# Optimization experiments

Measured on AMD Instinct MI355X. Metric: run time of the kernel, lower is better.

The kernel has to match this reference:

```python
import jax, jax.numpy as jnp
import numpy as np

N_NODES = 100000
IN_C, HID_C, OUT_C = 128, 128, 64
N_EDGES, N_POS, N_NEG = 1600000, 200000, 200000
BN_EPS = 1e-5


def setup_inputs() -> dict:
    key = jax.random.key(0)
    ks = jax.random.split(key, 24)
    s = 0.05
    inp = {
        'x': jax.random.normal(ks[0], (N_NODES, IN_C), jnp.float32),
        'edge_index': jax.random.randint(ks[1], (2, N_EDGES), 0, N_NODES, jnp.int64 if jax.config.jax_enable_x64 else jnp.int32),
        'pos_edge_index': jax.random.randint(ks[2], (2, N_POS), 0, N_NODES, jnp.int32),
        'neg_edge_index': jax.random.randint(ks[3], (2, N_NEG), 0, N_NODES, jnp.int32),
        # SAGEConv layer 1 (in->hid): lin_l (bias) on aggregated neighbors, lin_r (no bias) on root
        'Wl1': jax.random.normal(ks[4], (IN_C, HID_C), jnp.float32) * s,
        'bl1': jnp.zeros((HID_C,), jnp.float32),
        'Wr1': jax.random.normal(ks[5], (IN_C, HID_C), jnp.float32) * s,
        'g1': jnp.ones((HID_C,), jnp.float32),
        'b1': jnp.zeros((HID_C,), jnp.float32),
        # SAGEConv layer 2 (hid->hid)
        'Wl2': jax.random.normal(ks[6], (HID_C, HID_C), jnp.float32) * s,
        'bl2': jnp.zeros((HID_C,), jnp.float32),
        'Wr2': jax.random.normal(ks[7], (HID_C, HID_C), jnp.float32) * s,
        'g2': jnp.ones((HID_C,), jnp.float32),
        'b2': jnp.zeros((HID_C,), jnp.float32),
        # SAGEConv layer 3 (hid->out)
        'Wl3': jax.random.normal(ks[8], (HID_C, OUT_C), jnp.float32) * s,
        'bl3': jnp.zeros((OUT_C,), jnp.float32),
        'Wr3': jax.random.normal(ks[9], (HID_C, OUT_C), jnp.float32) * s,
        # edge predictor: Linear(2*out, hid) -> ReLU -> Linear(hid, 1)
        'We1': jax.random.normal(ks[10], (2 * OUT_C, HID_C), jnp.float32) * s,
        'be1': jnp.zeros((HID_C,), jnp.float32),
        'We2': jax.random.normal(ks[11], (HID_C, 1), jnp.float32) * s,
        'be2': jnp.zeros((1,), jnp.float32),
    }
    return inp


def _sage_conv(x, src, dst, Wl, bl, Wr):
    # mean aggregation of source features at destination nodes (PyG SAGEConv default)
    msg = x[src]                                                   # [E, C] gather
    agg = jax.ops.segment_sum(msg, dst, num_segments=N_NODES)      # [N, C] scatter-add
    deg = jax.ops.segment_sum(jnp.ones((src.shape[0],), x.dtype), dst, num_segments=N_NODES)
    mean = agg / jnp.maximum(deg, 1.0)[:, None]
    return mean @ Wl + bl + x @ Wr


def _bn_eval(x, gamma, beta):
    # BatchNorm1d eval mode with init running stats (mean 0, var 1)
    return x * (gamma / jnp.sqrt(1.0 + BN_EPS)) + beta


def _encode(x, edge_index, Wl1, bl1, Wr1, g1, b1, Wl2, bl2, Wr2, g2, b2, Wl3, bl3, Wr3):
    src, dst = edge_index[0], edge_index[1]
    h = x
    # layer 1 (+ residual: in_channels == hidden_channels)
    h1 = jax.nn.relu(_bn_eval(_sage_conv(h, src, dst, Wl1, bl1, Wr1), g1, b1))
    h = h1 + h if h.shape[1] == h1.shape[1] else h1
    # layer 2 (+ residual)
    h2 = jax.nn.relu(_bn_eval(_sage_conv(h, src, dst, Wl2, bl2, Wr2), g2, b2))
    h = h2 + h
    # output layer (no norm/relu/residual)
    return _sage_conv(h, src, dst, Wl3, bl3, Wr3)


def _decode(z, edge_index, We1, be1, We2, be2):
    s, d = edge_index[0], edge_index[1]
    ef = jnp.concatenate([z[s], z[d]], axis=-1)           # [E, 2*OUT_C]
    hidden = jax.nn.relu(ef @ We1 + be1)
    return jax.nn.sigmoid((hidden @ We2 + be2)[:, 0])


def reference(x, edge_index, pos_edge_index, neg_edge_index,
              Wl1, bl1, Wr1, g1, b1, Wl2, bl2, Wr2, g2, b2, Wl3, bl3, Wr3,
              We1, be1, We2, be2):
    z = _encode(x, edge_index, Wl1, bl1, Wr1, g1, b1, Wl2, bl2, Wr2, g2, b2, Wl3, bl3, Wr3)
    pos = _decode(z, pos_edge_index, We1, be1, We2, be2)
    neg = _decode(z, neg_edge_index, We1, be1, We2, be2)
    return (z, pos, neg)
```

## Files before the change

### kernel.cpp

```cpp
#include <hip/hip_runtime.h>
#include <hip/hip_bf16.h>

typedef unsigned short u16;
typedef unsigned char u8;
typedef short short8 __attribute__((ext_vector_type(8)));
typedef float floatx4 __attribute__((ext_vector_type(4)));
typedef float floatx2 __attribute__((ext_vector_type(2)));

__device__ __forceinline__ float b2f(u16 u) {
    unsigned v = ((unsigned)u) << 16;
    float f;
    __builtin_memcpy(&f, &v, 4);
    return f;
}
__device__ __forceinline__ float b2f_lo(unsigned w) { return b2f((u16)(w & 0xffffu)); }
__device__ __forceinline__ float b2f_hi(unsigned w) { return b2f((u16)(w >> 16)); }
__device__ __forceinline__ u16 f2b(float f) {
    unsigned u;
    __builtin_memcpy(&u, &f, 4);
    u = u + 0x7fffu + ((u >> 16) & 1u);
    return (u16)(u >> 16);
}
__device__ __forceinline__ unsigned pack2(float a, float b) {
    return (unsigned)f2b(a) | ((unsigned)f2b(b) << 16);
}
__device__ __forceinline__ float loadp(const void* p, int i, int f) {
    return f ? ((const float*)p)[i] : b2f(((const u16*)p)[i]);
}
__device__ __forceinline__ u8 f2e4m3(float v) {
    int r = __builtin_amdgcn_cvt_pk_fp8_f32(v, v, 0, false);
    return (u8)(r & 0xff);
}
__device__ __forceinline__ void acc16_fp8(float* a, uint4 p) {
    floatx2 f;
    f = __builtin_amdgcn_cvt_pk_f32_fp8((int)p.x, false); a[0] += f[0];  a[1] += f[1];
    f = __builtin_amdgcn_cvt_pk_f32_fp8((int)p.x, true);  a[2] += f[0];  a[3] += f[1];
    f = __builtin_amdgcn_cvt_pk_f32_fp8((int)p.y, false); a[4] += f[0];  a[5] += f[1];
    f = __builtin_amdgcn_cvt_pk_f32_fp8((int)p.y, true);  a[6] += f[0];  a[7] += f[1];
    f = __builtin_amdgcn_cvt_pk_f32_fp8((int)p.z, false); a[8] += f[0];  a[9] += f[1];
    f = __builtin_amdgcn_cvt_pk_f32_fp8((int)p.z, true);  a[10] += f[0]; a[11] += f[1];
    f = __builtin_amdgcn_cvt_pk_f32_fp8((int)p.w, false); a[12] += f[0]; a[13] += f[1];
    f = __builtin_amdgcn_cvt_pk_f32_fp8((int)p.w, true);  a[14] += f[0]; a[15] += f[1];
}

__global__ void sniff_kernel(const unsigned* __restrict__ xw, const int* __restrict__ eiw,
                             int* __restrict__ flags) {
    __shared__ int s_fp32, s_i64;
    if (threadIdx.x == 0) { s_fp32 = 0; s_i64 = 1; }
    __syncthreads();
    int t = threadIdx.x;
    unsigned w = xw[t];
    float lo = b2f_lo(w);
    if (!(fabsf(lo) <= 64.0f)) atomicOr(&s_fp32, 1);
    if (eiw[2 * t + 1] != 0) atomicAnd(&s_i64, 0);
    __syncthreads();
    if (t == 0) { flags[0] = s_fp32; flags[1] = s_i64; }
}

__global__ void cvt_x_kernel(const void* __restrict__ x, u16* __restrict__ xb,
                             u16* __restrict__ x8,
                             const int* __restrict__ flags, int nPairs) {
    int f = flags[0];
    int i = blockIdx.x * 256 + threadIdx.x;
    if (i >= nPairs) return;
    float lo, hi;
    if (f) {
        float2 v = ((const float2*)x)[i];
        lo = v.x; hi = v.y;
        ((unsigned*)xb)[i] = pack2(lo, hi);
    } else {
        unsigned w = ((const unsigned*)x)[i];
        lo = b2f_lo(w); hi = b2f_hi(w);
        ((unsigned*)xb)[i] = w;
    }
    int r = __builtin_amdgcn_cvt_pk_fp8_f32(lo, hi, 0, false);
    x8[i] = (u16)(r & 0xffff);
}

__global__ void prep_all_kernel(const void* Wl1, const void* Wr1, u16* __restrict__ W1t,
                                const void* Wl2, const void* Wr2, u16* __restrict__ W2t,
                                const void* Wl3, const void* Wr3, u16* __restrict__ W3t,
                                const void* We1, u16* __restrict__ Webt,
                                const void* g1, const void* b1, const void* bl1,
                                float* __restrict__ al1, float* __restrict__ bt1,
                                const void* g2, const void* b2, const void* bl2,
                                float* __restrict__ al2, float* __restrict__ bt2,
                                const void* bl3,
                                float* __restrict__ al3, float* __restrict__ bt3,
                                const void* be1, const void* We2, const void* be2,
                                float* __restrict__ dparams,
                                const int* __restrict__ flags) {
    int f = flags[0];
    int idx = blockIdx.x * 256 + threadIdx.x;
    if (idx < 32768) {
        int n = idx >> 8, k = idx & 255;
        const void* src = (k < 128) ? Wl1 : Wr1;
        int j = (k & 127) * 128 + n;
        W1t[idx] = f ? f2b(((const float*)src)[j]) : ((const u16*)src)[j];
    } else if (idx < 65536) {
        int i = idx - 32768;
        int n = i >> 8, k = i & 255;
        const void* src = (k < 128) ? Wl2 : Wr2;
        int j = (k & 127) * 128 + n;
        W2t[i] = f ? f2b(((const float*)src)[j]) : ((const u16*)src)[j];
    } else if (idx < 81920) {
        int i = idx - 65536;
        int n = i >> 7, k = i & 127;
        const void* src = (n < 64) ? Wl3 : Wr3;
        int j = k * 64 + (n & 63);
        W3t[i] = f ? f2b(((const float*)src)[j]) : ((const u16*)src)[j];
    } else if (idx < 98304) {
        int i = idx - 81920;
        int n = i >> 7, k = i & 127;
        int j = k * 128 + n;
        Webt[i] = f ? f2b(((const float*)We1)[j]) : ((const u16*)We1)[j];
    } else {
        int i = idx - 98304;
        if (i < 128) {
            float s = loadp(g1, i, f) * rsqrtf(1.0f + 1e-5f);
            al1[i] = s;
            bt1[i] = loadp(bl1, i, f) * s + loadp(b1, i, f);
        } else if (i < 256) {
            int j = i - 128;
            float s = loadp(g2, j, f) * rsqrtf(1.0f + 1e-5f);
            al2[j] = s;
            bt2[j] = loadp(bl2, j, f) * s + loadp(b2, j, f);
        } else if (i < 384) {
            int j = i - 256;
            al3[j] = 1.0f;
            bt3[j] = (j < 64) ? 0.0f : loadp(bl3, j - 64, f);
        } else if (i < 512) {
            int j = i - 384;
            dparams[j] = loadp(be1, j, f);
            dparams[128 + j] = loadp(We2, j, f);
            if (j == 0) dparams[256] = loadp(be2, 0, f);
        }
    }
}

__device__ __forceinline__ int edge_at(const int* ei, long long idx, int i64) {
    return i64 ? ei[2 * idx] : ei[idx];
}

__global__ __launch_bounds__(256) void bucket_count_kernel(const int* __restrict__ ei,
                                                           int* __restrict__ blockhist,
                                                           int E, int EPB, int B1, int nbuck,
                                                           const int* __restrict__ flags) {
    __shared__ int hist[1024];
    for (int i = threadIdx.x; i < nbuck; i += 256) hist[i] = 0;
    __syncthreads();
    int i64 = flags[1];
    int b = blockIdx.x;
    int lo = b * EPB, hi = min(lo + EPB, E);
    for (int e = lo + (int)threadIdx.x; e < hi; e += 256) {
        int d = edge_at(ei, (long long)E + e, i64);
        atomicAdd(&hist[d >> 7], 1);
    }
    __syncthreads();
    for (int k = threadIdx.x; k < nbuck; k += 256)
        blockhist[(size_t)k * B1 + b] = hist[k];
}

__global__ __launch_bounds__(64) void colscan_kernel(int* __restrict__ blockhist,
                                                     int* __restrict__ coltot, int B1) {
    int k = blockIdx.x, l = threadIdx.x;
    int* bh = blockhist + (size_t)k * B1;
    int x0 = (l < B1) ? bh[l] : 0;
    int x1 = (64 + l < B1) ? bh[64 + l] : 0;
    int s0 = x0;
    #pragma unroll
    for (int off = 1; off < 64; off <<= 1) {
        int u = __shfl_up(s0, off, 64);
        if (l >= off) s0 += u;
    }
    int tot0 = __shfl(s0, 63, 64);
    int s1 = x1;
    #pragma unroll
    for (int off = 1; off < 64; off <<= 1) {
        int u = __shfl_up(s1, off, 64);
        if (l >= off) s1 += u;
    }
    int tot1 = __shfl(s1, 63, 64);
    s1 += tot0;
    if (l < B1) bh[l] = s0 - x0;
    if (64 + l < B1) bh[64 + l] = s1 - x1;
    if (l == 0) coltot[k] = tot0 + tot1;
}

__global__ __launch_bounds__(1024) void base_scan_kernel(const int* __restrict__ coltot,
                                                         int* __restrict__ bucketbase,
                                                         int* __restrict__ rowptrN,
                                                         int nbuck, int E) {
    __shared__ int wsum[16];
    int t = threadIdx.x, lane = t & 63, w = t >> 6;
    int v = (t < nbuck) ? coltot[t] : 0;
    int inc = v;
    #pragma unroll
    for (int off = 1; off < 64; off <<= 1) {
        int u = __shfl_up(inc, off, 64);
        if (lane >= off) inc += u;
    }
    if (lane == 63) wsum[w] = inc;
    __syncthreads();
    int add = 0;
    for (int i = 0; i < w; ++i) add += wsum[i];
    if (t < nbuck) bucketbase[t] = add + inc - v;
    if (t == 0) rowptrN[0] = E;
}

__global__ __launch_bounds__(256) void bucket_scatter_kernel(const int* __restrict__ ei,
                                                             const int* __restrict__ bucketbase,
                                                             const int* __restrict__ blockhist,
                                                             int2* __restrict__ pairs,
                                                             int E, int EPB, int B1, int nbuck,
                                                             const int* __restrict__ flags) {
    __shared__ int off[1024];
    int b = blockIdx.x;
    for (int k = threadIdx.x; k < nbuck; k += 256)
        off[k] = bucketbase[k] + blockhist[(size_t)k * B1 + b];
    __syncthreads();
    int i64 = flags[1];
    int lo = b * EPB, hi = min(lo + EPB, E);
    for (int e = lo + (int)threadIdx.x; e < hi; e += 256) {
        int s = edge_at(ei, e, i64);
        int d = edge_at(ei, (long long)E + e, i64);
        int slot = atomicAdd(&off[d >> 7], 1);
        pairs[slot] = make_int2(s, d);
    }
}

__global__ __launch_bounds__(256) void bucket_csr_kernel(const int2* __restrict__ pairs,
                                                         const int* __restrict__ bucketbase,
                                                         const int* __restrict__ coltot,
                                                         int* __restrict__ rowptr,
                                                         int* __restrict__ col, int N) {
    __shared__ int srcs[4096];
    __shared__ unsigned char dl[4096];
    __shared__ int hist[128], cur[128];
    int k = blockIdx.x, tid = threadIdx.x;
    if (tid < 128) hist[tid] = 0;
    __syncthreads();
    int base = bucketbase[k], cnt = coltot[k];
    int staged = min(cnt, 4096);
    for (int i = tid; i < cnt; i += 256) {
        int2 pr = pairs[base + i];
        int j = pr.y & 127;
        atomicAdd(&hist[j], 1);
        if (i < 4096) { srcs[i] = pr.x; dl[i] = (unsigned char)j; }
    }
    __syncthreads();
    if (tid < 64) {
        int x0 = hist[tid], x1 = hist[64 + tid];
        int s0 = x0;
        #pragma unroll
        for (int off = 1; off < 64; off <<= 1) {
            int u = __shfl_up(s0, off, 64);
            if (tid >= off) s0 += u;
        }
        int tot0 = __shfl(s0, 63, 64);
        int s1 = x1;
        #pragma unroll
        for (int off = 1; off < 64; off <<= 1) {
            int u = __shfl_up(s1, off, 64);
            if (tid >= off) s1 += u;
        }
        s1 += tot0;
        cur[tid] = s0 - x0;
        cur[64 + tid] = s1 - x1;
    }
    __syncthreads();
    int node0 = k << 7;
    if (tid < 128 && node0 + tid < N) rowptr[node0 + tid] = base + cur[tid];
    __syncthreads();
    for (int i = tid; i < staged; i += 256) {
        int slot = base + atomicAdd(&cur[dl[i]], 1);
        col[slot] = srcs[i];
    }
    for (int i = 4096 + tid; i < cnt; i += 256) {
        int2 pr = pairs[base + i];
        int slot = base + atomicAdd(&cur[pr.y & 127], 1);
        col[slot] = pr.x;
    }
}

template <int CH>
__global__ __launch_bounds__(256) void aggregate_fp8_kernel(const u8* __restrict__ X8,
                                                            const int* __restrict__ rowptr,
                                                            const int* __restrict__ col,
                                                            u16* __restrict__ meanout, int N) {
    constexpr int LPR = CH / 16;
    constexpr int GPB = 256 / LPR;
    int t = threadIdx.x;
    int g = t / LPR;
    int o = t % LPR;
    int u = blockIdx.x * GPB + g;
    if (u >= N) return;
    const uint4* Xv = (const uint4*)X8;
    int beg = rowptr[u], end = rowptr[u + 1];
    float a[16];
    #pragma unroll
    for (int i = 0; i < 16; ++i) a[i] = 0.f;
    int e = beg;
    for (; e + 4 <= end; e += 4) {
        int c0 = col[e], c1 = col[e + 1], c2 = col[e + 2], c3 = col[e + 3];
        uint4 p0 = Xv[(size_t)c0 * LPR + o];
        uint4 p1 = Xv[(size_t)c1 * LPR + o];
        uint4 p2 = Xv[(size_t)c2 * LPR + o];
        uint4 p3 = Xv[(size_t)c3 * LPR + o];
        acc16_fp8(a, p0); acc16_fp8(a, p1); acc16_fp8(a, p2); acc16_fp8(a, p3);
    }
    for (; e < end; ++e) {
        uint4 p = Xv[(size_t)col[e] * LPR + o];
        acc16_fp8(a, p);
    }
    int deg = end - beg;
    float inv = (deg > 0) ? 1.0f / (float)deg : 0.0f;
    uint4 ov0, ov1;
    ov0.x = pack2(a[0] * inv, a[1] * inv);   ov0.y = pack2(a[2] * inv, a[3] * inv);
    ov0.z = pack2(a[4] * inv, a[5] * inv);   ov0.w = pack2(a[6] * inv, a[7] * inv);
    ov1.x = pack2(a[8] * inv, a[9] * inv);   ov1.y = pack2(a[10] * inv, a[11] * inv);
    ov1.z = pack2(a[12] * inv, a[13] * inv); ov1.w = pack2(a[14] * inv, a[15] * inv);
    uint4* mo = (uint4*)meanout;
    mo[(size_t)u * (CH / 8) + o * 2 + 0] = ov0;
    mo[(size_t)u * (CH / 8) + o * 2 + 1] = ov1;
}

__global__ __launch_bounds__(256) void agg_combine_kernel(const u8* __restrict__ T8,
                                                          const int* __restrict__ rowptr,
                                                          const int* __restrict__ col,
                                                          const u16* __restrict__ ubuf,
                                                          u16* __restrict__ zbuf,
                                                          void* __restrict__ dout,
                                                          int N, const int* __restrict__ flags) {
    constexpr int LPR = 4;
    constexpr int GPB = 64;
    int f = flags[0];
    int t = threadIdx.x;
    int g = t / LPR;
    int o = t % LPR;
    int u = blockIdx.x * GPB + g;
    if (u >= N) return;
    const uint4* Xv = (const uint4*)T8;
    int beg = rowptr[u], end = rowptr[u + 1];
    float a[16];
    #pragma unroll
    for (int i = 0; i < 16; ++i) a[i] = 0.f;
    int e = beg;
    for (; e + 4 <= end; e += 4) {
        int c0 = col[e], c1 = col[e + 1], c2 = col[e + 2], c3 = col[e + 3];
        uint4 p0 = Xv[(size_t)c0 * LPR + o];
        uint4 p1 = Xv[(size_t)c1 * LPR + o];
        uint4 p2 = Xv[(size_t)c2 * LPR + o];
        uint4 p3 = Xv[(size_t)c3 * LPR + o];
        acc16_fp8(a, p0); acc16_fp8(a, p1); acc16_fp8(a, p2); acc16_fp8(a, p3);
    }
    for (; e < end; ++e) {
        uint4 p = Xv[(size_t)col[e] * LPR + o];
        acc16_fp8(a, p);
    }
    int deg = end - beg;
    float inv = (deg > 0) ? 1.0f / (float)deg : 0.0f;
    const uint4* uv = (const uint4*)(ubuf + (size_t)u * 64 + o * 16);
    uint4 u0 = uv[0], u1 = uv[1];
    float z[16];
    z[0] = a[0] * inv + b2f_lo(u0.x);  z[1] = a[1] * inv + b2f_hi(u0.x);
    z[2] = a[2] * inv + b2f_lo(u0.y);  z[3] = a[3] * inv + b2f_hi(u0.y);
    z[4] = a[4] * inv + b2f_lo(u0.z);  z[5] = a[5] * inv + b2f_hi(u0.z);
    z[6] = a[6] * inv + b2f_lo(u0.w);  z[7] = a[7] * inv + b2f_hi(u0.w);
    z[8] = a[8] * inv + b2f_lo(u1.x);  z[9] = a[9] * inv + b2f_hi(u1.x);
    z[10] = a[10] * inv + b2f_lo(u1.y); z[11] = a[11] * inv + b2f_hi(u1.y);
    z[12] = a[12] * inv + b2f_lo(u1.z); z[13] = a[13] * inv + b2f_hi(u1.z);
    z[14] = a[14] * inv + b2f_lo(u1.w); z[15] = a[15] * inv + b2f_hi(u1.w);
    uint4 zv0, zv1;
    zv0.x = pack2(z[0], z[1]);   zv0.y = pack2(z[2], z[3]);
    zv0.z = pack2(z[4], z[5]);   zv0.w = pack2(z[6], z[7]);
    zv1.x = pack2(z[8], z[9]);   zv1.y = pack2(z[10], z[11]);
    zv1.z = pack2(z[12], z[13]); zv1.w = pack2(z[14], z[15]);
    uint4* zo = (uint4*)(zbuf + (size_t)u * 64 + o * 16);
    zo[0] = zv0; zo[1] = zv1;
    if (f) {
        float* fo = (float*)dout + (size_t)u * 64 + o * 16;
        #pragma unroll
        for (int i = 0; i < 16; ++i) fo[i] = z[i];
    } else {
        uint4* bo = (uint4*)((u16*)dout + (size_t)u * 64 + o * 16);
        bo[0] = zv0; bo[1] = zv1;
    }
}

template <int K>
__global__ __launch_bounds__(256) void gemm_sage_kernel(
    const u16* __restrict__ A1, const u16* __restrict__ A2,
    const u16* __restrict__ Wt,
    const float* __restrict__ alpha, const float* __restrict__ beta,
    int addRes, u16* __restrict__ out, int ldo, u16* __restrict__ outB,
    u8* __restrict__ out8, int ld8,
    int M, int relu) {
    int tid = threadIdx.x;
    int mBase = blockIdx.x * 64, nBase = blockIdx.y * 64;
    int lane = tid & 63, w = tid >> 6;
    int wm = w >> 1, wn = w & 1;
    int q = lane >> 4, r = lane & 15;

    floatx4 acc[2][2];
    #pragma unroll
    for (int mi = 0; mi < 2; ++mi)
        #pragma unroll
        for (int ni = 0; ni < 2; ++ni)
            acc[mi][ni] = (floatx4){0.f, 0.f, 0.f, 0.f};

    int row0 = mBase + wm * 32 + r;
    int row1 = row0 + 16;
    int r0c = min(row0, M - 1), r1c = min(row1, M - 1);
    const u16* bp = Wt + (size_t)(nBase + wn * 32 + r) * K + q * 8;

    #pragma unroll
    for (int k0 = 0; k0 < K; k0 += 32) {
        const u16* Abase = (k0 < 128) ? (A1 + k0) : (A2 + (k0 - 128));
        short8 af0 = *(const short8*)(Abase + (size_t)r0c * 128 + q * 8);
        short8 af1 = *(const short8*)(Abase + (size_t)r1c * 128 + q * 8);
        short8 bf0 = *(const short8*)(bp + k0);
        short8 bf1 = *(const short8*)(bp + 16 * K + k0);
        acc[0][0] = __builtin_amdgcn_mfma_f32_16x16x32_bf16(af0, bf0, acc[0][0], 0, 0, 0);
        acc[0][1] = __builtin_amdgcn_mfma_f32_16x16x32_bf16(af0, bf1, acc[0][1], 0, 0, 0);
        acc[1][0] = __builtin_amdgcn_mfma_f32_16x16x32_bf16(af1, bf0, acc[1][0], 0, 0, 0);
        acc[1][1] = __builtin_amdgcn_mfma_f32_16x16x32_bf16(af1, bf1, acc[1][1], 0, 0, 0);
    }

    #pragma unroll
    for (int mi = 0; mi < 2; ++mi)
        #pragma unroll
        for (int ni = 0; ni < 2; ++ni) {
            int colv = nBase + wn * 32 + ni * 16 + r;
            float al = alpha[colv], be = beta[colv];
            #pragma unroll
            for (int r4 = 0; r4 < 4; ++r4) {
                int row = mBase + wm * 32 + mi * 16 + q * 4 + r4;
                if (row < M) {
                    float v = acc[mi][ni][r4] * al + be;
                    if (relu) v = fmaxf(v, 0.0f);
                    if (addRes) v += b2f(A2[(size_t)row * 128 + colv]);
                    if (outB) {
                        if (colv < 64) out8[(size_t)row * 64 + colv] = f2e4m3(v);
                        else outB[(size_t)row * 64 + (colv - 64)] = f2b(v);
                    } else {
                        out[(size_t)row * ldo + colv] = f2b(v);
                        if (out8) out8[(size_t)row * ld8 + colv] = f2e4m3(v);
                    }
                }
            }
        }
}

__global__ __launch_bounds__(256) void decode_kernel(
    const u16* __restrict__ z,
    const int* __restrict__ sidx, const int* __restrict__ didx,
    const u16* __restrict__ Webt,
    const float* __restrict__ dparams,
    void* __restrict__ dout, long long outBase, int nE,
    const int* __restrict__ flags) {
    __shared__ u16 As[64 * 136];
    __shared__ float red[4][32];
    __shared__ float be1f[128], We2f[128];
    int tid = threadIdx.x;
    int f = flags[0];

    if (tid < 128) { be1f[tid] = dparams[tid]; We2f[tid] = dparams[128 + tid]; }

    int eBase = blockIdx.x * 64;
    {
        int row = tid >> 2, ch = tid & 3;
        int e = eBase + row;
        if (e >= nE) e = nE - 1;
        int node = (ch < 2) ? sidx[e] : didx[e];
        int off = (ch & 1) * 32;
        const short8* src = (const short8*)(z + (size_t)node * 64 + off);
        #pragma unroll
        for (int j = 0; j < 4; ++j)
            *(short8*)(&As[row * 136 + ch * 32 + j * 8]) = src[j];
    }
    __syncthreads();

    int lane = tid & 63, w = tid >> 6;
    int wm = w >> 1, wn = w & 1;
    int q = lane >> 4, r = lane & 15;
    floatx4 acc[2][4];
    #pragma unroll
    for (int mi = 0; mi < 2; ++mi)
        #pragma unroll
        for (int ni = 0; ni < 4; ++ni)
            acc[mi][ni] = (floatx4){0.f, 0.f, 0.f, 0.f};

    const u16* bp = Webt + (size_t)(wn * 64 + r) * 128 + q * 8;
    #pragma unroll
    for (int k0 = 0; k0 < 128; k0 += 32) {
        short8 af[2], bfv[4];
        #pragma unroll
        for (int mi = 0; mi < 2; ++mi)
            af[mi] = *(const short8*)(&As[(wm * 32 + mi * 16 + r) * 136 + k0 + q * 8]);
        #pragma unroll
        for (int ni = 0; ni < 4; ++ni)
            bfv[ni] = *(const short8*)(bp + (size_t)ni * 16 * 128 + k0);
        #pragma unroll
        for (int mi = 0; mi < 2; ++mi)
            #pragma unroll
            for (int ni = 0; ni < 4; ++ni)
                acc[mi][ni] = __builtin_amdgcn_mfma_f32_16x16x32_bf16(af[mi], bfv[ni], acc[mi][ni], 0, 0, 0);
    }

    float part[2][4] = {{0.f, 0.f, 0.f, 0.f}, {0.f, 0.f, 0.f, 0.f}};
    #pragma unroll
    for (int mi = 0; mi < 2; ++mi)
        #pragma unroll
        for (int ni = 0; ni < 4; ++ni) {
            int colv = wn * 64 + ni * 16 + r;
            float bb = be1f[colv], mm = We2f[colv];
            #pragma unroll
            for (int r4 = 0; r4 < 4; ++r4) {
                float v = acc[mi][ni][r4] + bb;
                part[mi][r4] += fmaxf(v, 0.0f) * mm;
            }
        }
    #pragma unroll
    for (int mi = 0; mi < 2; ++mi)
        #pragma unroll
        for (int r4 = 0; r4 < 4; ++r4) {
            float v = part[mi][r4];
            v += __shfl_xor(v, 1, 64);
            v += __shfl_xor(v, 2, 64);
            v += __shfl_xor(v, 4, 64);
            v += __shfl_xor(v, 8, 64);
            part[mi][r4] = v;
        }
    if (r == 0) {
        #pragma unroll
        for (int mi = 0; mi < 2; ++mi)
            #pragma unroll
            for (int r4 = 0; r4 < 4; ++r4)
                red[w][mi * 16 + q * 4 + r4] = part[mi][r4];
    }
    __syncthreads();
    if (tid < 64) {
        int e = eBase + tid;
        if (e < nE) {
            int half = tid >> 5, loc = tid & 31;
            float s = red[half * 2 + 0][loc] + red[half * 2 + 1][loc] + dparams[256];
            float sg = 1.0f / (1.0f + expf(-s));
            if (f) ((float*)dout)[outBase + e] = sg;
            else   ((u16*)dout)[outBase + e] = f2b(sg);
        }
    }
}


extern "C" void kernel_launch(void* const* d_in, const int* in_sizes, int n_in,
                              void* d_out, int out_size, void* d_ws, size_t ws_size,
                              hipStream_t stream) {
    const void* x   = d_in[0];
    const int* ei   = (const int*)d_in[1];
    const int* pos  = (const int*)d_in[2];
    const int* neg  = (const int*)d_in[3];
    const void* Wl1 = d_in[4];
    const void* bl1 = d_in[5];
    const void* Wr1 = d_in[6];
    const void* g1  = d_in[7];
    const void* b1  = d_in[8];
    const void* Wl2 = d_in[9];
    const void* bl2 = d_in[10];
    const void* Wr2 = d_in[11];
    const void* g2  = d_in[12];
    const void* b2  = d_in[13];
    const void* Wl3 = d_in[14];
    const void* bl3 = d_in[15];
    const void* Wr3 = d_in[16];
    const void* We1 = d_in[17];
    const void* be1 = d_in[18];
    const void* We2 = d_in[19];
    const void* be2 = d_in[20];

    const int N = in_sizes[0] / 128;
    const int E = in_sizes[1] / 2;
    const int nPos = in_sizes[2] / 2;
    const int nNeg = in_sizes[3] / 2;
    const int nbuck = (N + 127) >> 7;
    const int EPB = (((E + 95) / 96) + 3) & ~3;
    const int B1 = (E + EPB - 1) / EPB;

    char* p = (char*)d_ws;
    auto alloc = [&](size_t bytes) -> void* {
        void* r = (void*)p;
        p += (bytes + 255) & ~(size_t)255;
        return r;
    };
    int*   flags     = (int*)alloc(64);
    int*   blockhist = (int*)alloc((size_t)nbuck * B1 * 4);
    int*   coltot    = (int*)alloc((size_t)nbuck * 4);
    int*   bucketbase= (int*)alloc((size_t)nbuck * 4);
    int*   rowptr    = (int*)alloc((size_t)(N + 1) * 4);
    int2*  pairs     = (int2*)alloc((size_t)E * 8);
    int*   colbuf    = (int*)alloc((size_t)E * 4);
    u16*   xb      = (u16*)alloc((size_t)N * 128 * 2);
    u16*   hbufA   = (u16*)alloc((size_t)N * 128 * 2);
    u16*   meanbuf = (u16*)alloc((size_t)N * 128 * 2);
    u8*    x8      = (u8*)alloc((size_t)N * 128);
    u8*    h8      = (u8*)alloc((size_t)N * 128);
    u8*    t8      = (u8*)alloc((size_t)N * 64);
    u16*   W1t     = (u16*)alloc((size_t)128 * 256 * 2);
    u16*   W2t     = (u16*)alloc((size_t)128 * 256 * 2);
    u16*   W3t     = (u16*)alloc((size_t)128 * 128 * 2);
    u16*   Webt    = (u16*)alloc((size_t)128 * 128 * 2);
    float* al1 = (float*)alloc(128 * 4);
    float* bt1 = (float*)alloc(128 * 4);
    float* al2 = (float*)alloc(128 * 4);
    float* bt2 = (float*)alloc(128 * 4);
    float* al3 = (float*)alloc(128 * 4);
    float* bt3 = (float*)alloc(128 * 4);
    float* dparams = (float*)alloc(260 * 4);
    u16* hbufB = xb;
    u16* ubuf  = meanbuf + (size_t)N * 64;
    u16* zbuf  = hbufA + (size_t)N * 64;

    sniff_kernel<<<1, 256, 0, stream>>>((const unsigned*)x, ei, flags);
    bucket_count_kernel<<<B1, 256, 0, stream>>>(ei, blockhist, E, EPB, B1, nbuck, flags);
    colscan_kernel<<<nbuck, 64, 0, stream>>>(blockhist, coltot, B1);
    base_scan_kernel<<<1, 1024, 0, stream>>>(coltot, bucketbase, rowptr + N, nbuck, E);
    bucket_scatter_kernel<<<B1, 256, 0, stream>>>(ei, bucketbase, blockhist, pairs, E, EPB, B1, nbuck, flags);
    bucket_csr_kernel<<<nbuck, 256, 0, stream>>>(pairs, bucketbase, coltot, rowptr, colbuf, N);

    cvt_x_kernel<<<(N * 64 + 255) / 256, 256, 0, stream>>>(x, xb, (u16*)x8, flags, N * 64);
    prep_all_kernel<<<(98816 + 255) / 256, 256, 0, stream>>>(
        Wl1, Wr1, W1t, Wl2, Wr2, W2t, Wl3, Wr3, W3t, We1, Webt,
        g1, b1, bl1, al1, bt1, g2, b2, bl2, al2, bt2, bl3, al3, bt3,
        be1, We2, be2, dparams, flags);

    dim3 gemmGrid2((N + 63) / 64, 2);

    aggregate_fp8_kernel<128><<<(N + 31) / 32, 256, 0, stream>>>(x8, rowptr, colbuf, meanbuf, N);
    gemm_sage_kernel<256><<<gemmGrid2, 256, 0, stream>>>(meanbuf, xb, W1t, al1, bt1,
                                                         1, hbufA, 128, nullptr, h8, 128, N, 1);
    aggregate_fp8_kernel<128><<<(N + 31) / 32, 256, 0, stream>>>(h8, rowptr, colbuf, meanbuf, N);
    gemm_sage_kernel<256><<<gemmGrid2, 256, 0, stream>>>(meanbuf, hbufA, W2t, al2, bt2,
                                                         1, hbufB, 128, nullptr, nullptr, 0, N, 1);
    gemm_sage_kernel<128><<<gemmGrid2, 256, 0, stream>>>(hbufB, hbufB, W3t, al3, bt3,
                                                         0, nullptr, 0, ubuf, t8, 64, N, 0);
    agg_combine_kernel<<<(N + 63) / 64, 256, 0, stream>>>(t8, rowptr, colbuf, ubuf, zbuf,
                                                          d_out, N, flags);

    long long posBase = (long long)N * 64;
    long long negBase = posBase + nPos;
    decode_kernel<<<(nPos + 63) / 64, 256, 0, stream>>>(zbuf, pos, pos + nPos, Webt, dparams,
                                                        d_out, posBase, nPos, flags);
    decode_kernel<<<(nNeg + 63) / 64, 256, 0, stream>>>(zbuf, neg, neg + nNeg, Webt, dparams,
                                                        d_out, negBase, nNeg, flags);
}
```

Measured before the change: 550.9 us.

## Stage GEMM tiles in LDS and compute full 128-column output per block

The SAGE GEMM kernel now loads 64xK A tiles and 128-row weight tiles into shared memory per 32-wide k-step, and each block computes all 128 output columns instead of splitting N across two grid blocks. This removes the duplicate A reads from global memory that came from the two N-blocks, and shares operand loads across waves. In exchange it adds two barriers per k-step with no double buffering, drops the unrolled direct-to-register loads, and halves the grid size.

```diff
diff --git a/kernel.cpp b/kernel.cpp
--- a/kernel.cpp
+++ b/kernel.cpp
@@ -388,6 +388,7 @@
     }
 }
 
+#define LDA 40
 template <int K>
 __global__ __launch_bounds__(256) void gemm_sage_kernel(
     const u16* __restrict__ A1, const u16* __restrict__ A2,
@@ -396,42 +397,48 @@
     int addRes, u16* __restrict__ out, int ldo, u16* __restrict__ outB,
     u8* __restrict__ out8, int ld8,
     int M, int relu) {
+    __shared__ u16 As[64 * LDA];
+    __shared__ u16 Bs[128 * LDA];
     int tid = threadIdx.x;
-    int mBase = blockIdx.x * 64, nBase = blockIdx.y * 64;
+    int mBase = blockIdx.x * 64;
     int lane = tid & 63, w = tid >> 6;
     int wm = w >> 1, wn = w & 1;
     int q = lane >> 4, r = lane & 15;
 
-    floatx4 acc[2][2];
+    floatx4 acc[2][4];
     #pragma unroll
     for (int mi = 0; mi < 2; ++mi)
         #pragma unroll
-        for (int ni = 0; ni < 2; ++ni)
+        for (int ni = 0; ni < 4; ++ni)
             acc[mi][ni] = (floatx4){0.f, 0.f, 0.f, 0.f};
 
-    int row0 = mBase + wm * 32 + r;
-    int row1 = row0 + 16;
-    int r0c = min(row0, M - 1), r1c = min(row1, M - 1);
-    const u16* bp = Wt + (size_t)(nBase + wn * 32 + r) * K + q * 8;
-
-    #pragma unroll
+    int rowA = tid >> 2, kcA = (tid & 3) * 8;
+    int grA = min(mBase + rowA, M - 1);
+    int nB = tid >> 1, kcB = (tid & 1) * 16;
+
     for (int k0 = 0; k0 < K; k0 += 32) {
         const u16* Abase = (k0 < 128) ? (A1 + k0) : (A2 + (k0 - 128));
-        short8 af0 = *(const short8*)(Abase + (size_t)r0c * 128 + q * 8);
-        short8 af1 = *(const short8*)(Abase + (size_t)r1c * 128 + q * 8);
-        short8 bf0 = *(const short8*)(bp + k0);
-        short8 bf1 = *(const short8*)(bp + 16 * K + k0);
-        acc[0][0] = __builtin_amdgcn_mfma_f32_16x16x32_bf16(af0, bf0, acc[0][0], 0, 0, 0);
-        acc[0][1] = __builtin_amdgcn_mfma_f32_16x16x32_bf16(af0, bf1, acc[0][1], 0, 0, 0);
-        acc[1][0] = __builtin_amdgcn_mfma_f32_16x16x32_bf16(af1, bf0, acc[1][0], 0, 0, 0);
-        acc[1][1] = __builtin_amdgcn_mfma_f32_16x16x32_bf16(af1, bf1, acc[1][1], 0, 0, 0);
+        *(short8*)(&As[rowA * LDA + kcA]) = *(const short8*)(Abase + (size_t)grA * 128 + kcA);
+        const u16* bsrc = Wt + (size_t)nB * K + k0 + kcB;
+        *(short8*)(&Bs[nB * LDA + kcB]) = *(const short8*)bsrc;
+        *(short8*)(&Bs[nB * LDA + kcB + 8]) = *(const short8*)(bsrc + 8);
+        __syncthreads();
+        short8 af0 = *(const short8*)(&As[(wm * 32 + r) * LDA + q * 8]);
+        short8 af1 = *(const short8*)(&As[(wm * 32 + 16 + r) * LDA + q * 8]);
+        #pragma unroll
+        for (int ni = 0; ni < 4; ++ni) {
+            short8 bf = *(const short8*)(&Bs[(wn * 64 + ni * 16 + r) * LDA + q * 8]);
+            acc[0][ni] = __builtin_amdgcn_mfma_f32_16x16x32_bf16(af0, bf, acc[0][ni], 0, 0, 0);
+            acc[1][ni] = __builtin_amdgcn_mfma_f32_16x16x32_bf16(af1, bf, acc[1][ni], 0, 0, 0);
+        }
+        __syncthreads();
     }
 
     #pragma unroll
     for (int mi = 0; mi < 2; ++mi)
         #pragma unroll
-        for (int ni = 0; ni < 2; ++ni) {
-            int colv = nBase + wn * 32 + ni * 16 + r;
+        for (int ni = 0; ni < 4; ++ni) {
+            int colv = wn * 64 + ni * 16 + r;
             float al = alpha[colv], be = beta[colv];
             #pragma unroll
             for (int r4 = 0; r4 < 4; ++r4) {
@@ -633,16 +640,16 @@
         g1, b1, bl1, al1, bt1, g2, b2, bl2, al2, bt2, bl3, al3, bt3,
         be1, We2, be2, dparams, flags);
 
-    dim3 gemmGrid2((N + 63) / 64, 2);
+    int gemmGrid = (N + 63) / 64;
 
     aggregate_fp8_kernel<128><<<(N + 31) / 32, 256, 0, stream>>>(x8, rowptr, colbuf, meanbuf, N);
-    gemm_sage_kernel<256><<<gemmGrid2, 256, 0, stream>>>(meanbuf, xb, W1t, al1, bt1,
-                                                         1, hbufA, 128, nullptr, h8, 128, N, 1);
+    gemm_sage_kernel<256><<<gemmGrid, 256, 0, stream>>>(meanbuf, xb, W1t, al1, bt1,
+                                                        1, hbufA, 128, nullptr, h8, 128, N, 1);
     aggregate_fp8_kernel<128><<<(N + 31) / 32, 256, 0, stream>>>(h8, rowptr, colbuf, meanbuf, N);
-    gemm_sage_kernel<256><<<gemmGrid2, 256, 0, stream>>>(meanbuf, hbufA, W2t, al2, bt2,
-                                                         1, hbufB, 128, nullptr, nullptr, 0, N, 1);
-    gemm_sage_kernel<128><<<gemmGrid2, 256, 0, stream>>>(hbufB, hbufB, W3t, al3, bt3,
-                                                         0, nullptr, 0, ubuf, t8, 64, N, 0);
+    gemm_sage_kernel<256><<<gemmGrid, 256, 0, stream>>>(meanbuf, hbufA, W2t, al2, bt2,
+                                                        1, hbufB, 128, nullptr, nullptr, 0, N, 1);
+    gemm_sage_kernel<128><<<gemmGrid, 256, 0, stream>>>(hbufB, hbufB, W3t, al3, bt3,
+                                                        0, nullptr, 0, ubuf, t8, 64, N, 0);
     agg_combine_kernel<<<(N + 63) / 64, 256, 0, stream>>>(t8, rowptr, colbuf, ubuf, zbuf,
                                                           d_out, N, flags);
 
```

After: 502.4 us. 8.8% less time.
